# Kernel optimization log

Measured on AMD Instinct MI355X. Metric: run time of the kernel, lower is better.

## Reference

```python
import jax, jax.numpy as jnp
import numpy as np

N_NODES = 100000
N_EDGES = 1000000
D_MODEL = 128
EDGE_DIM = 64
LN_EPS = 1e-5


def _layernorm(x, gamma, beta, eps=LN_EPS):
    mu = jnp.mean(x, axis=-1, keepdims=True)
    var = jnp.var(x, axis=-1, keepdims=True)
    return (x - mu) * jax.lax.rsqrt(var + eps) * gamma + beta


def setup_inputs() -> dict:
    key = jax.random.key(0)
    ks = jax.random.split(key, 12)
    std = 1.0 / np.sqrt(D_MODEL)
    stde = 1.0 / np.sqrt(EDGE_DIM)
    return {
        "x_src": jax.random.normal(ks[0], (N_NODES, D_MODEL), jnp.float32),
        "x_dst": jax.random.normal(ks[1], (N_NODES, D_MODEL), jnp.float32),
        "edge_attr": jax.random.normal(ks[2], (N_EDGES, EDGE_DIM), jnp.float32),
        "edge_index": jax.random.randint(ks[3], (2, N_EDGES), 0, N_NODES, jnp.int32),
        # params
        "W_src": jax.random.uniform(ks[4], (D_MODEL, D_MODEL), jnp.float32, -std, std),
        "W_dst": jax.random.uniform(ks[5], (D_MODEL, D_MODEL), jnp.float32, -std, std),
        "b_dst": jnp.zeros((D_MODEL,), jnp.float32),
        "Wg1": jax.random.uniform(ks[6], (EDGE_DIM, D_MODEL), jnp.float32, -stde, stde),
        "bg1": jnp.zeros((D_MODEL,), jnp.float32),
        "Wg2": jax.random.uniform(ks[7], (D_MODEL, 1), jnp.float32, -std, std),
        "bg2": jnp.zeros((1,), jnp.float32),
        "gamma": jnp.ones((D_MODEL,), jnp.float32),
        "beta": jnp.zeros((D_MODEL,), jnp.float32),
    }


def reference(x_src, x_dst, edge_attr, edge_index,
              W_src, W_dst, b_dst, Wg1, bg1, Wg2, bg2, gamma, beta):
    s, d = edge_index[0], edge_index[1]
    n = x_dst.shape[0]
    # gather + linear (no bias): [E, D]
    msg = x_src[s] @ W_src
    # edge gate MLP: Linear -> gelu -> Linear (no norm, eval so no dropout)
    h = jax.nn.gelu(edge_attr @ Wg1 + bg1, approximate=False)
    gate = jax.nn.sigmoid(h @ Wg2 + bg2)  # [E, 1]
    msg = msg * gate
    # scatter-add aggregate + mean by in-degree (clamped at 1)
    out = jax.ops.segment_sum(msg, d, num_segments=n)
    deg = jax.ops.segment_sum(jnp.ones((msg.shape[0],), msg.dtype), d, num_segments=n)
    out = out / jnp.clip(deg, 1.0)[:, None]
    # residual-like combine, layernorm, gelu
    out = _layernorm(out + x_dst @ W_dst + b_dst, gamma, beta)
    return jax.nn.gelu(out, approximate=False)
```

## Files before the change

kernel.cpp:

```cpp
#include <hip/hip_runtime.h>
#include <hip/hip_fp16.h>
#include <math.h>

#define N_NODES 100000
#define N_EDGES 1000000
#define D_MODEL 128
#define EDGE_DIM 64
#define SCHUNK 250
#define NSB 400

typedef short bf16x8 __attribute__((ext_vector_type(8)));
typedef float f32x4 __attribute__((ext_vector_type(4)));

__device__ __forceinline__ short f2bf(float f) {
    union { float f; unsigned u; } v; v.f = f;
    unsigned r = v.u + 0x7FFFu + ((v.u >> 16) & 1u);
    return (short)(r >> 16);
}
__device__ __forceinline__ float gelu_fast(float x) {
    float t = 0.7978845608028654f * x * (1.0f + 0.044715f * x * x);
    float e = __expf(2.0f * t);
    return x * (1.0f - __builtin_amdgcn_rcpf(e + 1.0f));
}
__device__ __forceinline__ float sigmoid_fast(float x) {
    return __builtin_amdgcn_rcpf(1.0f + __expf(-x));
}
__device__ __forceinline__ float bflo(unsigned v) { return __uint_as_float(v << 16); }
__device__ __forceinline__ float bfhi(unsigned v) { return __uint_as_float(v & 0xFFFF0000u); }

__global__ __launch_bounds__(256) void k_zero_int(int* __restrict__ p, int n) {
    int i = blockIdx.x * 256 + threadIdx.x;
    if (i < n) p[i] = 0;
}

__global__ __launch_bounds__(256) void k_prep(
    const float* __restrict__ Ws, const float* __restrict__ Wd,
    const float* __restrict__ Wg1, short* __restrict__ frag)
{
    int g = blockIdx.x * 256 + threadIdx.x;
    if (g >= 5120) return;
    const float* W; short* T; int q;
    if (g < 2048)      { W = Ws;  T = frag;         q = g; }
    else if (g < 4096) { W = Wd;  T = frag + 16384; q = g - 2048; }
    else               { W = Wg1; T = frag + 32768; q = g - 4096; }
    int ls = q & 63, nt = (q >> 6) & 7, kb = q >> 9;
    int col = nt * 16 + (ls & 15);
    int k0 = kb * 32 + (ls >> 4) * 8;
    bf16x8 v;
    #pragma unroll
    for (int e = 0; e < 8; ++e) v[e] = f2bf(W[(k0 + e) * D_MODEL + col]);
    *reinterpret_cast<bf16x8*>(T + (size_t)q * 8) = v;
}

__global__ __launch_bounds__(256, 2) void k_node_linear(
    const float* __restrict__ x_src, const float* __restrict__ x_dst,
    const short* __restrict__ WsrcF, const short* __restrict__ WdstF,
    const float* __restrict__ b_dst,
    short* __restrict__ ysrc, float* __restrict__ z)
{
    __shared__ __align__(16) short Bf[4][8][64][8];
    const int tid = threadIdx.x;
    const int lane = tid & 63;
    const int wid = tid >> 6;
    const int l15 = lane & 15;
    const int lg = lane >> 4;
    const int mat = blockIdx.y;
    const float* __restrict__ X = mat ? x_dst : x_src;
    const short* __restrict__ WF = mat ? WdstF : WsrcF;
    const int row0 = blockIdx.x * 128 + wid * 32;

    float4 av[4][2][2];
    #pragma unroll
    for (int kb = 0; kb < 4; ++kb)
        #pragma unroll
        for (int st = 0; st < 2; ++st) {
            int r = min(row0 + st * 16 + l15, N_NODES - 1);
            const float* p = X + (size_t)r * D_MODEL + kb * 32 + lg * 8;
            av[kb][st][0] = *reinterpret_cast<const float4*>(p);
            av[kb][st][1] = *reinterpret_cast<const float4*>(p + 4);
        }
    #pragma unroll
    for (int i = 0; i < 8; ++i)
        reinterpret_cast<int4*>(Bf)[tid + i * 256] =
            reinterpret_cast<const int4*>(WF)[tid + i * 256];
    __syncthreads();

    bf16x8 a[4][2];
    #pragma unroll
    for (int kb = 0; kb < 4; ++kb)
        #pragma unroll
        for (int st = 0; st < 2; ++st) {
            float4 v0 = av[kb][st][0], v1 = av[kb][st][1];
            bf16x8 t;
            t[0] = f2bf(v0.x); t[1] = f2bf(v0.y); t[2] = f2bf(v0.z); t[3] = f2bf(v0.w);
            t[4] = f2bf(v1.x); t[5] = f2bf(v1.y); t[6] = f2bf(v1.z); t[7] = f2bf(v1.w);
            a[kb][st] = t;
        }

    f32x4 acc[2][8];
    #pragma unroll
    for (int st = 0; st < 2; ++st)
        #pragma unroll
        for (int nt = 0; nt < 8; ++nt) { f32x4 zz = {0.f,0.f,0.f,0.f}; acc[st][nt] = zz; }

    #pragma unroll
    for (int kb = 0; kb < 4; ++kb)
        #pragma unroll
        for (int nt = 0; nt < 8; ++nt) {
            bf16x8 b = *reinterpret_cast<const bf16x8*>(&Bf[kb][nt][lane][0]);
            acc[0][nt] = __builtin_amdgcn_mfma_f32_16x16x32_bf16(a[kb][0], b, acc[0][nt], 0, 0, 0);
            acc[1][nt] = __builtin_amdgcn_mfma_f32_16x16x32_bf16(a[kb][1], b, acc[1][nt], 0, 0, 0);
        }

    #pragma unroll
    for (int st = 0; st < 2; ++st) {
        int rowb = row0 + st * 16 + lg * 4;
        #pragma unroll
        for (int nt = 0; nt < 8; ++nt) {
            int col = nt * 16 + l15;
            float bias = mat ? b_dst[col] : 0.0f;
            #pragma unroll
            for (int r = 0; r < 4; ++r) {
                int row = rowb + r;
                if (row < N_NODES) {
                    float v = acc[st][nt][r];
                    if (mat) z[(size_t)row * D_MODEL + col] = v + bias;
                    else     ysrc[(size_t)row * D_MODEL + col] = f2bf(v);
                }
            }
        }
    }
}

__global__ __launch_bounds__(256, 4) void k_gate(
    const float* __restrict__ ea, const short* __restrict__ Wg1F,
    const float* __restrict__ bg1, const float* __restrict__ Wg2,
    const float* __restrict__ bg2, __half* __restrict__ gate_h)
{
    __shared__ __align__(16) short Bf[2][8][64][8];
    const int tid = threadIdx.x;
    const int lane = tid & 63;
    const int wid = tid >> 6;
    const int l15 = lane & 15;
    const int lg = lane >> 4;
    const int e0 = blockIdx.x * 128 + wid * 32;

    float4 av[2][2][2];
    #pragma unroll
    for (int kb = 0; kb < 2; ++kb)
        #pragma unroll
        for (int st = 0; st < 2; ++st) {
            int r = min(e0 + st * 16 + l15, N_EDGES - 1);
            const float* p = ea + (size_t)r * EDGE_DIM + kb * 32 + lg * 8;
            av[kb][st][0] = *reinterpret_cast<const float4*>(p);
            av[kb][st][1] = *reinterpret_cast<const float4*>(p + 4);
        }
    float b1v[2][4], w2v[2][4];
    #pragma unroll
    for (int ntc = 0; ntc < 2; ++ntc)
        #pragma unroll
        for (int nt = 0; nt < 4; ++nt) {
            int col = (ntc * 4 + nt) * 16 + l15;
            b1v[ntc][nt] = bg1[col];
            w2v[ntc][nt] = Wg2[col];
        }
    #pragma unroll
    for (int i = 0; i < 4; ++i)
        reinterpret_cast<int4*>(Bf)[tid + i * 256] =
            reinterpret_cast<const int4*>(Wg1F)[tid + i * 256];
    __syncthreads();

    bf16x8 a[2][2];
    #pragma unroll
    for (int kb = 0; kb < 2; ++kb)
        #pragma unroll
        for (int st = 0; st < 2; ++st) {
            float4 v0 = av[kb][st][0], v1 = av[kb][st][1];
            bf16x8 t;
            t[0] = f2bf(v0.x); t[1] = f2bf(v0.y); t[2] = f2bf(v0.z); t[3] = f2bf(v0.w);
            t[4] = f2bf(v1.x); t[5] = f2bf(v1.y); t[6] = f2bf(v1.z); t[7] = f2bf(v1.w);
            a[kb][st] = t;
        }

    float part[2][4] = {{0.f,0.f,0.f,0.f},{0.f,0.f,0.f,0.f}};
    #pragma unroll
    for (int ntc = 0; ntc < 2; ++ntc) {
        f32x4 acc[2][4];
        #pragma unroll
        for (int st = 0; st < 2; ++st)
            #pragma unroll
            for (int nt = 0; nt < 4; ++nt) { f32x4 zz = {0.f,0.f,0.f,0.f}; acc[st][nt] = zz; }
        #pragma unroll
        for (int kb = 0; kb < 2; ++kb)
            #pragma unroll
            for (int nt = 0; nt < 4; ++nt) {
                bf16x8 b = *reinterpret_cast<const bf16x8*>(&Bf[kb][ntc * 4 + nt][lane][0]);
                acc[0][nt] = __builtin_amdgcn_mfma_f32_16x16x32_bf16(a[kb][0], b, acc[0][nt], 0, 0, 0);
                acc[1][nt] = __builtin_amdgcn_mfma_f32_16x16x32_bf16(a[kb][1], b, acc[1][nt], 0, 0, 0);
            }
        #pragma unroll
        for (int nt = 0; nt < 4; ++nt) {
            float b1 = b1v[ntc][nt], w2 = w2v[ntc][nt];
            #pragma unroll
            for (int st = 0; st < 2; ++st)
                #pragma unroll
                for (int r = 0; r < 4; ++r)
                    part[st][r] += gelu_fast(acc[st][nt][r] + b1) * w2;
        }
    }

    #pragma unroll
    for (int m = 1; m <= 8; m <<= 1)
        #pragma unroll
        for (int st = 0; st < 2; ++st)
            #pragma unroll
            for (int r = 0; r < 4; ++r)
                part[st][r] += __shfl_xor(part[st][r], m);

    if (l15 == 0) {
        float b2 = bg2[0];
        #pragma unroll
        for (int st = 0; st < 2; ++st)
            #pragma unroll
            for (int r = 0; r < 4; ++r) {
                int e = e0 + st * 16 + lg * 4 + r;
                if (e < N_EDGES) gate_h[e] = __float2half(sigmoid_fast(part[st][r] + b2));
            }
    }
}

__global__ void k_deg(const int* __restrict__ dst, int* __restrict__ deg) {
    int e = blockIdx.x * 256 + threadIdx.x;
    if (e < N_EDGES) atomicAdd(&deg[dst[e]], 1);
}
__global__ __launch_bounds__(256) void k_scan1(const int* __restrict__ deg, int* __restrict__ bsum) {
    __shared__ int s[256];
    int tid = threadIdx.x;
    int i = blockIdx.x * SCHUNK + tid;
    int v = (tid < SCHUNK && i < N_NODES) ? deg[i] : 0;
    s[tid] = v; __syncthreads();
    for (int off = 128; off > 0; off >>= 1) {
        if (tid < off) s[tid] += s[tid + off];
        __syncthreads();
    }
    if (tid == 0) bsum[blockIdx.x] = s[0];
}
__global__ __launch_bounds__(512) void k_scan2(const int* __restrict__ bsum, int* __restrict__ boff) {
    __shared__ int s[512];
    int tid = threadIdx.x;
    int v = (tid < NSB) ? bsum[tid] : 0;
    s[tid] = v; __syncthreads();
    for (int off = 1; off < 512; off <<= 1) {
        int t = (tid >= off) ? s[tid - off] : 0;
        __syncthreads();
        s[tid] += t;
        __syncthreads();
    }
    if (tid < NSB) boff[tid] = s[tid] - v;
}
__global__ __launch_bounds__(256) void k_scan3(const int* __restrict__ deg, const int* __restrict__ boff,
                                               int* __restrict__ cursor) {
    __shared__ int s[256];
    int tid = threadIdx.x;
    int i = blockIdx.x * SCHUNK + tid;
    int v = (tid < SCHUNK && i < N_NODES) ? deg[i] : 0;
    s[tid] = v; __syncthreads();
    for (int off = 1; off < 256; off <<= 1) {
        int t = (tid >= off) ? s[tid - off] : 0;
        __syncthreads();
        s[tid] += t;
        __syncthreads();
    }
    int excl = s[tid] - v;
    if (tid < SCHUNK && i < N_NODES) cursor[i] = boff[blockIdx.x] + excl;
}
__global__ void k_fill(const int* __restrict__ dst, const int* __restrict__ srcI,
                       const unsigned short* __restrict__ gate_h, int* __restrict__ cursor,
                       int* __restrict__ sg_s, unsigned short* __restrict__ sg_g) {
    int e = blockIdx.x * 256 + threadIdx.x;
    if (e < N_EDGES) {
        int d = dst[e];
        int p = atomicAdd(&cursor[d], 1);
        sg_s[p] = srcI[e];
        sg_g[p] = gate_h[e];
    }
}

__global__ __launch_bounds__(256) void k_agg(
    const int* __restrict__ cursorEnd, const int* __restrict__ deg,
    const int* __restrict__ sg_s, const __half* __restrict__ sg_g,
    const short* __restrict__ ysrc, const float* __restrict__ z,
    const float* __restrict__ gamma, const float* __restrict__ beta,
    float* __restrict__ out)
{
    const int lane = threadIdx.x & 63;
    const int wid = threadIdx.x >> 6;
    const int n = blockIdx.x * 4 + wid;
    const int dg = deg[n];
    const int start = cursorEnd[n] - dg;
    const int c0 = lane * 2;

    float a0 = 0.f, a1 = 0.f;
    int t = 0;
    for (; t + 4 <= dg; t += 4) {
        int s0 = sg_s[start + t + 0];
        int s1 = sg_s[start + t + 1];
        int s2 = sg_s[start + t + 2];
        int s3 = sg_s[start + t + 3];
        float g0 = __half2float(sg_g[start + t + 0]);
        float g1 = __half2float(sg_g[start + t + 1]);
        float g2 = __half2float(sg_g[start + t + 2]);
        float g3 = __half2float(sg_g[start + t + 3]);
        unsigned p0 = *reinterpret_cast<const unsigned*>(&ysrc[(size_t)s0 * D_MODEL + c0]);
        unsigned p1 = *reinterpret_cast<const unsigned*>(&ysrc[(size_t)s1 * D_MODEL + c0]);
        unsigned p2 = *reinterpret_cast<const unsigned*>(&ysrc[(size_t)s2 * D_MODEL + c0]);
        unsigned p3 = *reinterpret_cast<const unsigned*>(&ysrc[(size_t)s3 * D_MODEL + c0]);
        a0 += g0 * bflo(p0) + g1 * bflo(p1) + g2 * bflo(p2) + g3 * bflo(p3);
        a1 += g0 * bfhi(p0) + g1 * bfhi(p1) + g2 * bfhi(p2) + g3 * bfhi(p3);
    }
    for (; t < dg; ++t) {
        int s0 = sg_s[start + t];
        float g0 = __half2float(sg_g[start + t]);
        unsigned p0 = *reinterpret_cast<const unsigned*>(&ysrc[(size_t)s0 * D_MODEL + c0]);
        a0 += g0 * bflo(p0);
        a1 += g0 * bfhi(p0);
    }

    float inv = 1.0f / fmaxf((float)dg, 1.0f);
    float2 zv = *reinterpret_cast<const float2*>(&z[(size_t)n * D_MODEL + c0]);
    float t0 = a0 * inv + zv.x;
    float t1 = a1 * inv + zv.y;

    float sum = t0 + t1;
    #pragma unroll
    for (int m = 1; m <= 32; m <<= 1) sum += __shfl_xor(sum, m);
    float mu = sum * (1.0f / 128.0f);
    float d0 = t0 - mu, d1 = t1 - mu;
    float vs = d0 * d0 + d1 * d1;
    #pragma unroll
    for (int m = 1; m <= 32; m <<= 1) vs += __shfl_xor(vs, m);
    float rstd = rsqrtf(vs * (1.0f / 128.0f) + 1e-5f);

    float2 gv = *reinterpret_cast<const float2*>(&gamma[c0]);
    float2 bv = *reinterpret_cast<const float2*>(&beta[c0]);
    float o0 = d0 * rstd * gv.x + bv.x;
    float o1 = d1 * rstd * gv.y + bv.y;
    float2 o = make_float2(gelu_fast(o0), gelu_fast(o1));
    *reinterpret_cast<float2*>(&out[(size_t)n * D_MODEL + c0]) = o;
}

extern "C" void kernel_launch(void* const* d_in, const int* in_sizes, int n_in,
                              void* d_out, int out_size, void* d_ws, size_t ws_size,
                              hipStream_t stream)
{
    const float* x_src = (const float*)d_in[0];
    const float* x_dst = (const float*)d_in[1];
    const float* ea    = (const float*)d_in[2];
    const int*   ei    = (const int*)d_in[3];
    const float* W_src = (const float*)d_in[4];
    const float* W_dst = (const float*)d_in[5];
    const float* b_dst = (const float*)d_in[6];
    const float* Wg1   = (const float*)d_in[7];
    const float* bg1   = (const float*)d_in[8];
    const float* Wg2   = (const float*)d_in[9];
    const float* bg2   = (const float*)d_in[10];
    const float* gamma = (const float*)d_in[11];
    const float* beta  = (const float*)d_in[12];
    const int* srcIdx = ei;
    const int* dstIdx = ei + N_EDGES;

    char* ws = (char*)d_ws;
    short*  fragT  = (short*)(ws);
    short*  ysrc   = (short*)(ws + 81920);
    float*  z      = (float*)(ws + 25681920);
    __half* gate_h = (__half*)(ws + 76881920);
    int*    deg    = (int*)(ws + 78881920);
    int*    cursor = (int*)(ws + 79281920);
    int*    sg_s   = (int*)(ws + 79681920);
    unsigned short* sg_g = (unsigned short*)(ws + 83681920);
    int*    bsum   = (int*)(ws + 85681920);
    int*    boff   = (int*)(ws + 85683520);

    float* out = (float*)d_out;

    hipLaunchKernelGGL(k_zero_int, dim3((N_NODES + 255) / 256), dim3(256), 0, stream, deg, N_NODES);
    hipLaunchKernelGGL(k_prep, dim3(20), dim3(256), 0, stream, W_src, W_dst, Wg1, fragT);
    hipLaunchKernelGGL(k_node_linear, dim3(782, 2), dim3(256), 0, stream,
                       x_src, x_dst, fragT, fragT + 16384, b_dst, ysrc, z);
    hipLaunchKernelGGL(k_gate, dim3(7813), dim3(256), 0, stream,
                       ea, fragT + 32768, bg1, Wg2, bg2, gate_h);
    hipLaunchKernelGGL(k_deg, dim3(3907), dim3(256), 0, stream, dstIdx, deg);
    hipLaunchKernelGGL(k_scan1, dim3(NSB), dim3(256), 0, stream, deg, bsum);
    hipLaunchKernelGGL(k_scan2, dim3(1), dim3(512), 0, stream, bsum, boff);
    hipLaunchKernelGGL(k_scan3, dim3(NSB), dim3(256), 0, stream, deg, boff, cursor);
    hipLaunchKernelGGL(k_fill, dim3(3907), dim3(256), 0, stream,
                       dstIdx, srcIdx, (const unsigned short*)gate_h, cursor, sg_s, sg_g);
    hipLaunchKernelGGL(k_agg, dim3(N_NODES / 4), dim3(256), 0, stream,
                       cursor, deg, sg_s, (const __half*)sg_g, ysrc, z, gamma, beta, out);
}
```

Baseline: 308.6 us.

## Fuse CSR fill into gate kernel and store dst linear output in bf16

The edge gate kernel now does the atomic cursor fill directly, writing src index and gate into sorted slots. This removes the separate fill kernel and the intermediate gate array. The scan is moved before the gate kernel to make that possible. The node-dst linear output z is stored as bf16 instead of fp32, halving its write and read traffic, at some cost in precision before layernorm.

```diff
diff --git a/kernel.cpp b/kernel.cpp
--- a/kernel.cpp
+++ b/kernel.cpp
@@ -56,7 +56,7 @@
     const float* __restrict__ x_src, const float* __restrict__ x_dst,
     const short* __restrict__ WsrcF, const short* __restrict__ WdstF,
     const float* __restrict__ b_dst,
-    short* __restrict__ ysrc, float* __restrict__ z)
+    short* __restrict__ ysrc, short* __restrict__ z_bf)
 {
     __shared__ __align__(16) short Bf[4][8][64][8];
     const int tid = threadIdx.x;
@@ -124,7 +124,7 @@
                 int row = rowb + r;
                 if (row < N_NODES) {
                     float v = acc[st][nt][r];
-                    if (mat) z[(size_t)row * D_MODEL + col] = v + bias;
+                    if (mat) z_bf[(size_t)row * D_MODEL + col] = f2bf(v + bias);
                     else     ysrc[(size_t)row * D_MODEL + col] = f2bf(v);
                 }
             }
@@ -132,10 +132,13 @@
     }
 }
 
-__global__ __launch_bounds__(256, 4) void k_gate(
+__global__ __launch_bounds__(256, 4) void k_gate_fill(
     const float* __restrict__ ea, const short* __restrict__ Wg1F,
     const float* __restrict__ bg1, const float* __restrict__ Wg2,
-    const float* __restrict__ bg2, __half* __restrict__ gate_h)
+    const float* __restrict__ bg2,
+    const int* __restrict__ dstI, const int* __restrict__ srcI,
+    int* __restrict__ cursor, int* __restrict__ sg_s,
+    unsigned short* __restrict__ sg_g)
 {
     __shared__ __align__(16) short Bf[2][8][64][8];
     const int tid = threadIdx.x;
@@ -224,7 +227,15 @@
             #pragma unroll
             for (int r = 0; r < 4; ++r) {
                 int e = e0 + st * 16 + lg * 4 + r;
-                if (e < N_EDGES) gate_h[e] = __float2half(sigmoid_fast(part[st][r] + b2));
+                if (e < N_EDGES) {
+                    float gv = sigmoid_fast(part[st][r] + b2);
+                    int d = dstI[e];
+                    int s = srcI[e];
+                    int p = atomicAdd(&cursor[d], 1);
+                    __half h = __float2half(gv);
+                    sg_s[p] = s;
+                    sg_g[p] = *reinterpret_cast<unsigned short*>(&h);
+                }
             }
     }
 }
@@ -274,22 +285,11 @@
     int excl = s[tid] - v;
     if (tid < SCHUNK && i < N_NODES) cursor[i] = boff[blockIdx.x] + excl;
 }
-__global__ void k_fill(const int* __restrict__ dst, const int* __restrict__ srcI,
-                       const unsigned short* __restrict__ gate_h, int* __restrict__ cursor,
-                       int* __restrict__ sg_s, unsigned short* __restrict__ sg_g) {
-    int e = blockIdx.x * 256 + threadIdx.x;
-    if (e < N_EDGES) {
-        int d = dst[e];
-        int p = atomicAdd(&cursor[d], 1);
-        sg_s[p] = srcI[e];
-        sg_g[p] = gate_h[e];
-    }
-}
 
 __global__ __launch_bounds__(256) void k_agg(
     const int* __restrict__ cursorEnd, const int* __restrict__ deg,
     const int* __restrict__ sg_s, const __half* __restrict__ sg_g,
-    const short* __restrict__ ysrc, const float* __restrict__ z,
+    const short* __restrict__ ysrc, const short* __restrict__ z_bf,
     const float* __restrict__ gamma, const float* __restrict__ beta,
     float* __restrict__ out)
 {
@@ -327,9 +327,9 @@
     }
 
     float inv = 1.0f / fmaxf((float)dg, 1.0f);
-    float2 zv = *reinterpret_cast<const float2*>(&z[(size_t)n * D_MODEL + c0]);
-    float t0 = a0 * inv + zv.x;
-    float t1 = a1 * inv + zv.y;
+    unsigned zv = *reinterpret_cast<const unsigned*>(&z_bf[(size_t)n * D_MODEL + c0]);
+    float t0 = a0 * inv + bflo(zv);
+    float t1 = a1 * inv + bfhi(zv);
 
     float sum = t0 + t1;
     #pragma unroll
@@ -372,29 +372,26 @@
     char* ws = (char*)d_ws;
     short*  fragT  = (short*)(ws);
     short*  ysrc   = (short*)(ws + 81920);
-    float*  z      = (float*)(ws + 25681920);
-    __half* gate_h = (__half*)(ws + 76881920);
-    int*    deg    = (int*)(ws + 78881920);
-    int*    cursor = (int*)(ws + 79281920);
-    int*    sg_s   = (int*)(ws + 79681920);
-    unsigned short* sg_g = (unsigned short*)(ws + 83681920);
-    int*    bsum   = (int*)(ws + 85681920);
-    int*    boff   = (int*)(ws + 85683520);
+    short*  z_bf   = (short*)(ws + 25681920);
+    int*    deg    = (int*)(ws + 51281920);
+    int*    cursor = (int*)(ws + 51681920);
+    int*    sg_s   = (int*)(ws + 52081920);
+    unsigned short* sg_g = (unsigned short*)(ws + 56081920);
+    int*    bsum   = (int*)(ws + 58081920);
+    int*    boff   = (int*)(ws + 58083520);
 
     float* out = (float*)d_out;
 
     hipLaunchKernelGGL(k_zero_int, dim3((N_NODES + 255) / 256), dim3(256), 0, stream, deg, N_NODES);
-    hipLaunchKernelGGL(k_prep, dim3(20), dim3(256), 0, stream, W_src, W_dst, Wg1, fragT);
-    hipLaunchKernelGGL(k_node_linear, dim3(782, 2), dim3(256), 0, stream,
-                       x_src, x_dst, fragT, fragT + 16384, b_dst, ysrc, z);
-    hipLaunchKernelGGL(k_gate, dim3(7813), dim3(256), 0, stream,
-                       ea, fragT + 32768, bg1, Wg2, bg2, gate_h);
     hipLaunchKernelGGL(k_deg, dim3(3907), dim3(256), 0, stream, dstIdx, deg);
     hipLaunchKernelGGL(k_scan1, dim3(NSB), dim3(256), 0, stream, deg, bsum);
     hipLaunchKernelGGL(k_scan2, dim3(1), dim3(512), 0, stream, bsum, boff);
     hipLaunchKernelGGL(k_scan3, dim3(NSB), dim3(256), 0, stream, deg, boff, cursor);
-    hipLaunchKernelGGL(k_fill, dim3(3907), dim3(256), 0, stream,
-                       dstIdx, srcIdx, (const unsigned short*)gate_h, cursor, sg_s, sg_g);
+    hipLaunchKernelGGL(k_prep, dim3(20), dim3(256), 0, stream, W_src, W_dst, Wg1, fragT);
+    hipLaunchKernelGGL(k_node_linear, dim3(782, 2), dim3(256), 0, stream,
+                       x_src, x_dst, fragT, fragT + 16384, b_dst, ysrc, z_bf);
+    hipLaunchKernelGGL(k_gate_fill, dim3(7813), dim3(256), 0, stream,
+                       ea, fragT + 32768, bg1, Wg2, bg2, dstIdx, srcIdx, cursor, sg_s, sg_g);
     hipLaunchKernelGGL(k_agg, dim3(N_NODES / 4), dim3(256), 0, stream,
-                       cursor, deg, sg_s, (const __half*)sg_g, ysrc, z, gamma, beta, out);
-}
+                       cursor, deg, sg_s, (const __half*)sg_g, ysrc, z_bf, gamma, beta, out);
+}
```

Result: faster. 293.5 us (-4.9%).
